# Optimization experiments

Hardware: AMD Instinct MI355X
Metric: run time of the kernel (lower is better)

Reference implementation:

```python
import jax, jax.numpy as jnp
import numpy as np

B, M, K = 8, 2048, 64          # clouds, points per cloud, max neighbors
C_IN, C_OUT, R = 64, 64, 0.2   # channels, radius
BN_EPS = 1e-5                  # BatchNorm eval: running_mean=0, running_var=1


def _bn(y, g, b):
    # eval-mode BatchNorm1d with running stats (0, 1)
    return g * y * (1.0 / jnp.sqrt(1.0 + BN_EPS)) + b


def _lin_init(key, fan_in, shape):
    s = 1.0 / np.sqrt(fan_in)
    return jax.random.uniform(key, shape, jnp.float32, -s, s)


def setup_inputs() -> dict:
    key = jax.random.key(0)
    ks = jax.random.split(key, 16)
    N = B * M
    pos = jax.random.uniform(ks[0], (N, 3), jnp.float32)
    x = jax.random.normal(ks[1], (N, C_IN), jnp.float32)
    nrm = jax.random.normal(ks[2], (N, 3), jnp.float32)
    normal = nrm / jnp.linalg.norm(nrm, axis=-1, keepdims=True)
    batch = jnp.repeat(jnp.arange(B, dtype=jnp.int32), M)
    return {
        "x": x, "pos": pos, "normal": normal, "batch": batch,
        # PointTransformerConv linear layers (value / key / query)
        "lin_w": _lin_init(ks[3], C_IN, (C_IN, C_OUT)),
        "lin_b": _lin_init(ks[4], C_IN, (C_OUT,)),
        "lin_src_w": _lin_init(ks[5], C_IN, (C_IN, C_OUT)),
        "lin_src_b": _lin_init(ks[6], C_IN, (C_OUT,)),
        "lin_dst_w": _lin_init(ks[7], C_IN, (C_IN, C_OUT)),
        "lin_dst_b": _lin_init(ks[8], C_IN, (C_OUT,)),
        # pos_nn = MLP([6, C_OUT]): Linear -> BN -> ReLU (Dropout off in eval)
        "pos_w": _lin_init(ks[9], 6, (6, C_OUT)),
        "pos_b": _lin_init(ks[10], 6, (C_OUT,)),
        "pos_g": jnp.ones((C_OUT,), jnp.float32),
        "pos_bt": jnp.zeros((C_OUT,), jnp.float32),
        # attn_nn = MLP([C_OUT, C_OUT])
        "attn_w": _lin_init(ks[11], C_OUT, (C_OUT, C_OUT)),
        "attn_b": _lin_init(ks[12], C_OUT, (C_OUT,)),
        "attn_g": jnp.ones((C_OUT,), jnp.float32),
        "attn_bt": jnp.zeros((C_OUT,), jnp.float32),
    }


def _forward(x, pos, normal, lin_w, lin_b, lin_src_w, lin_src_b,
             lin_dst_w, lin_dst_b, pos_w, pos_b, pos_g, pos_bt,
             attn_w, attn_b, attn_g, attn_bt):
    xb = x.reshape(B, M, C_IN)
    pb = pos.reshape(B, M, 3)
    nb = normal.reshape(B, M, 3)

    # radius(pos, pos, r, batch, batch, max_num_neighbors=K):
    # per-cloud pairwise sq-distances -> K nearest, masked to d <= r.
    d2 = jnp.sum((pb[:, :, None, :] - pb[:, None, :, :]) ** 2, axis=-1)  # [B,M,M]
    neg_d2, idx = jax.lax.top_k(-d2, K)                                   # [B,M,K]
    mask = (-neg_d2) <= R * R                                             # self always valid

    gather = jax.vmap(lambda a, i: a[i])  # per-cloud gather: [M,C],[M,K] -> [M,K,C]

    v = xb @ lin_w + lin_b          # value   [B,M,C]
    kf = xb @ lin_src_w + lin_src_b # key     [B,M,C]
    q = xb @ lin_dst_w + lin_dst_b  # query   [B,M,C]

    vj = gather(v, idx)             # [B,M,K,C]
    kj = gather(kf, idx)
    pj = gather(pb, idx)            # [B,M,K,3]
    nj = gather(nb, idx)

    rel = jnp.concatenate([pb[:, :, None, :] - pj,
                           nb[:, :, None, :] - nj], axis=-1)  # [B,M,K,6]
    delta = jax.nn.relu(_bn(rel @ pos_w + pos_b, pos_g, pos_bt))  # [B,M,K,C]

    alpha = jax.nn.relu(_bn((q[:, :, None, :] - kj + delta) @ attn_w + attn_b,
                            attn_g, attn_bt))                     # [B,M,K,C]
    alpha = jnp.where(mask[..., None], alpha, -jnp.inf)
    w = jax.nn.softmax(alpha, axis=2)                              # softmax over neighbors

    out = jnp.sum(w * (vj + delta), axis=2)                        # [B,M,C]
    return out.reshape(B * M, C_OUT)


def reference(x, pos, normal, batch, lin_w, lin_b, lin_src_w, lin_src_b,
              lin_dst_w, lin_dst_b, pos_w, pos_b, pos_g, pos_bt,
              attn_w, attn_b, attn_g, attn_bt):
    del batch  # batch ids are block-contiguous: encoded by the [B,M] reshape
    return _forward(x, pos, normal, lin_w, lin_b, lin_src_w, lin_src_b,
                    lin_dst_w, lin_dst_b, pos_w, pos_b, pos_g, pos_bt,
                    attn_w, attn_b, attn_g, attn_bt)
```

## Files before the change

kernel.cpp:

```cpp
#include <hip/hip_runtime.h>
#include <math.h>

#define BB 8
#define MM 2048
#define KK 64
#define CC 64
#define NTOT (BB*MM)
#define R2 0.04f
#define CAP 256

typedef _Float16 h8 __attribute__((ext_vector_type(8)));
typedef _Float16 h4 __attribute__((ext_vector_type(4)));
typedef float f32x4 __attribute__((ext_vector_type(4)));

__device__ __forceinline__ int swz(int row, int col) {
  return (row << 6) + ((((col >> 3) ^ (row & 7)) << 3) | (col & 7));
}

__device__ __forceinline__ unsigned long long shfl_xor_u64(unsigned long long x, int off) {
  int lo = __shfl_xor((int)(unsigned)(x & 0xFFFFFFFFull), off, 64);
  int hi = __shfl_xor((int)(unsigned)(x >> 32), off, 64);
  return (((unsigned long long)(unsigned)hi) << 32) | (unsigned)lo;
}

__device__ __forceinline__ unsigned long long wave_min_u64(unsigned long long x) {
#pragma unroll
  for (int off = 32; off; off >>= 1) {
    unsigned long long o = shfl_xor_u64(x, off);
    x = (o < x) ? o : x;
  }
  return x;
}

__device__ __forceinline__ unsigned long long wave_max_u64(unsigned long long x) {
#pragma unroll
  for (int off = 32; off; off >>= 1) {
    unsigned long long o = shfl_xor_u64(x, off);
    x = (o > x) ? o : x;
  }
  return x;
}

__global__ __launch_bounds__(256) void prep_w(const float* __restrict__ attn_w,
                                              const float* __restrict__ pos_w,
                                              unsigned short* __restrict__ w_img,
                                              unsigned short* __restrict__ pw_img) {
  const int idx = blockIdx.x * 256 + threadIdx.x;
  if (idx < 4096) {
    const int d = idx >> 6, cc = idx & 63;
    const float v = attn_w[idx];
    w_img[swz(cc, d)] = __builtin_bit_cast(unsigned short, (_Float16)v);
  }
  if (idx < 64 * 24) {
    const int col = idx / 24, k = idx - col * 24;
    const float v = (k < 6) ? pos_w[k * 64 + col] : 0.f;
    pw_img[idx] = __builtin_bit_cast(unsigned short, (_Float16)v);
  }
}

__global__ __launch_bounds__(256) void proj_kernel(
    const float* __restrict__ x,
    const float* __restrict__ w0, const float* __restrict__ b0,
    const float* __restrict__ w1, const float* __restrict__ b1,
    const float* __restrict__ w2, const float* __restrict__ b2,
    float* __restrict__ o0, float* __restrict__ o1, float* __restrict__ o2) {
  __shared__ float xs[64 * 64];
  __shared__ float wss[64 * 64];
  const int tid = threadIdx.x;
  const int r0 = blockIdx.x << 6;
  const float* w; const float* bv; float* o;
  if (blockIdx.y == 0)      { w = w0; bv = b0; o = o0; }
  else if (blockIdx.y == 1) { w = w1; bv = b1; o = o1; }
  else                      { w = w2; bv = b2; o = o2; }
  for (int i = tid; i < 4096; i += 256) {
    xs[i]  = x[(size_t)r0 * 64 + i];
    wss[i] = w[i];
  }
  __syncthreads();
  const int c = tid & 63, rg = tid >> 6;
  float acc[16];
#pragma unroll
  for (int r = 0; r < 16; ++r) acc[r] = 0.f;
  for (int k = 0; k < 64; ++k) {
    const float wvv = wss[(k << 6) + c];
#pragma unroll
    for (int r = 0; r < 16; ++r)
      acc[r] = fmaf(xs[((rg * 16 + r) << 6) + k], wvv, acc[r]);
  }
  const float bb = bv[c];
#pragma unroll
  for (int r = 0; r < 16; ++r)
    o[(size_t)(r0 + rg * 16 + r) * 64 + c] = acc[r] + bb;
}

__global__ __launch_bounds__(256) void knn_kernel(const float* __restrict__ pos,
                                                  unsigned* __restrict__ nbr) {
  __shared__ float spos[MM * 3];
  __shared__ unsigned long long slist[4][CAP];
  const int bidx = blockIdx.x;
  const int b = bidx >> 9;
  const int qblk = bidx & 511;
  const int tid = threadIdx.x;
  const float* pc = pos + (size_t)b * MM * 3;
  for (int i = tid; i < MM * 3; i += 256) spos[i] = pc[i];
  __syncthreads();
  const int wv = tid >> 6, lane = tid & 63;
  const int q = (qblk << 2) + wv;
  const float qx = spos[q * 3 + 0], qy = spos[q * 3 + 1], qz = spos[q * 3 + 2];
  unsigned bits[32];
  unsigned cnt = 0;
#pragma unroll
  for (int i = 0; i < 32; ++i) {
    const int j = lane + (i << 6);
    const float dx = qx - spos[j * 3 + 0];
    const float dy = qy - spos[j * 3 + 1];
    const float dz = qz - spos[j * 3 + 2];
    const float d2 = __fadd_rn(__fadd_rn(__fmul_rn(dx, dx), __fmul_rn(dy, dy)), __fmul_rn(dz, dz));
    const unsigned bt = __float_as_uint(d2);
    bits[i] = bt;
    const bool val = (d2 <= R2);
    const unsigned long long mb = __ballot(val);
    if (val) {
      const unsigned off = cnt + (unsigned)__popcll(mb & ((1ull << lane) - 1ull));
      if (off < CAP) slist[wv][off] = (((unsigned long long)bt) << 32) | (unsigned)j;
    }
    cnt += (unsigned)__popcll(mb);
  }
  __syncthreads();
  unsigned outv;
  if (cnt <= 64u) {
    if (lane < (int)cnt) outv = ((unsigned)slist[wv][lane]) | 0x80000000u;
    else                 outv = 0u;
  } else if (cnt <= (unsigned)CAP) {
    unsigned long long s0, s1, s2, s3, t;
    s0 = (lane       < (int)cnt) ? slist[wv][lane      ] : ~0ull;
    s1 = (lane + 64  < (int)cnt) ? slist[wv][lane + 64 ] : ~0ull;
    s2 = (lane + 128 < (int)cnt) ? slist[wv][lane + 128] : ~0ull;
    s3 = (lane + 192 < (int)cnt) ? slist[wv][lane + 192] : ~0ull;
    if (s1 < s0) { t = s0; s0 = s1; s1 = t; }
    if (s3 < s2) { t = s2; s2 = s3; s3 = t; }
    if (s2 < s0) { t = s0; s0 = s2; s2 = t; }
    if (s3 < s1) { t = s1; s1 = s3; s3 = t; }
    if (s2 < s1) { t = s1; s1 = s2; s2 = t; }
    if (cnt <= 128u) {
      const int pops = (int)cnt - 64;
      int rl = (cnt > (unsigned)lane) ? (int)((cnt - (unsigned)lane + 63u) >> 6) : 0;
      if (rl > 4) rl = 4;
      int ti = rl - 1;
      for (int p = 0; p < pops; ++p) {
        const unsigned long long mx =
            (ti == 3) ? s3 : (ti == 2) ? s2 : (ti == 1) ? s1 : (ti == 0) ? s0 : 0ull;
        const unsigned long long g = wave_max_u64(mx);
        if (ti >= 0 && mx == g) ti--;
      }
      const int c = ti + 1;
      const unsigned long long b0 = __ballot(c & 1);
      const unsigned long long b1 = __ballot(c & 2);
      const unsigned long long b2 = __ballot(c & 4);
      const unsigned long long lm = (1ull << lane) - 1ull;
      const int pre = __popcll(b0 & lm) + 2 * __popcll(b1 & lm) + 4 * __popcll(b2 & lm);
      if (c > 0) slist[wv][pre + 0] = s0;
      if (c > 1) slist[wv][pre + 1] = s1;
      if (c > 2) slist[wv][pre + 2] = s2;
      if (c > 3) slist[wv][pre + 3] = s3;
      __asm volatile("s_waitcnt lgkmcnt(0)" ::: "memory");
      outv = ((unsigned)slist[wv][lane]) | 0x80000000u;
    } else {
      unsigned long long my = 0;
      for (int it = 0; it < 64; ++it) {
        const unsigned long long gg = wave_min_u64(s0);
        if (lane == it) my = gg;
        if (s0 == gg) { s0 = s1; s1 = s2; s2 = s3; s3 = ~0ull; }
      }
      outv = ((unsigned)my) | 0x80000000u;
    }
  } else {
    unsigned long long cur = ~0ull;
#pragma unroll
    for (int i = 0; i < 32; ++i) {
      const unsigned long long k = (((unsigned long long)bits[i]) << 32) | (unsigned)(lane + (i << 6));
      cur = (k < cur) ? k : cur;
    }
    unsigned long long my = 0;
    for (int it = 0; it < 64; ++it) {
      const unsigned long long gg = wave_min_u64(cur);
      if (lane == it) my = gg;
      if (cur == gg) {
        cur = ~0ull;
#pragma unroll
        for (int i = 0; i < 32; ++i) {
          const unsigned long long k = (((unsigned long long)bits[i]) << 32) | (unsigned)(lane + (i << 6));
          if (k > gg && k < cur) cur = k;
        }
      }
    }
    const float d2s = __uint_as_float((unsigned)(my >> 32));
    outv = ((unsigned)my) | ((d2s <= R2) ? 0x80000000u : 0u);
  }
  nbr[((size_t)(b * MM + q)) * 64 + lane] = outv;
}

__global__ __launch_bounds__(256, 4) void ptc_kernel(
    const float* __restrict__ pos, const float* __restrict__ nrm,
    const float* __restrict__ vv, const float* __restrict__ kf, const float* __restrict__ qq,
    const unsigned* __restrict__ nbr,
    const unsigned short* __restrict__ w_img, const unsigned short* __restrict__ pw_img,
    const float* __restrict__ pos_b, const float* __restrict__ pos_g, const float* __restrict__ pos_bt,
    const float* __restrict__ attn_b, const float* __restrict__ attn_g, const float* __restrict__ attn_bt,
    float* __restrict__ out) {
  __shared__ __align__(16) unsigned short s_w[4096];
  __shared__ __align__(16) unsigned short s_thi[4096];
  __shared__ __align__(16) unsigned short s_pw[64 * 24];
  __shared__ __align__(16) unsigned short s_relh[64 * 24];
  __shared__ unsigned s_sel[64];
  const int qi = blockIdx.x;
  const int b = qi >> 11;
  const int tid = threadIdx.x;
  const int wv = tid >> 6, lane = tid & 63;
  const int lrow = lane >> 4, lcol = lane & 15;
  const int col = (wv << 4) + lcol;
  const float bninv = 1.0f / sqrtf(1.0f + 1e-5f);

  {
    const uint4* wi = (const uint4*)w_img;
    uint4* sw = (uint4*)s_w;
#pragma unroll
    for (int i = 0; i < 2; ++i) sw[tid + 256 * i] = wi[tid + 256 * i];
    if (tid < 192) ((uint4*)s_pw)[tid] = ((const uint4*)pw_img)[tid];
  }
  if (tid < 64) {
    const unsigned s = nbr[(size_t)qi * 64 + tid];
    s_sel[tid] = s;
    const int j = (int)(s & 0x7FFFFFFFu);
    const int jg = (b << 11) + j;
    h8 hv;
    hv[0] = (_Float16)(pos[(size_t)qi * 3 + 0] - pos[(size_t)jg * 3 + 0]);
    hv[1] = (_Float16)(pos[(size_t)qi * 3 + 1] - pos[(size_t)jg * 3 + 1]);
    hv[2] = (_Float16)(pos[(size_t)qi * 3 + 2] - pos[(size_t)jg * 3 + 2]);
    hv[3] = (_Float16)(nrm[(size_t)qi * 3 + 0] - nrm[(size_t)jg * 3 + 0]);
    hv[4] = (_Float16)(nrm[(size_t)qi * 3 + 1] - nrm[(size_t)jg * 3 + 1]);
    hv[5] = (_Float16)(nrm[(size_t)qi * 3 + 2] - nrm[(size_t)jg * 3 + 2]);
    hv[6] = (_Float16)0.f; hv[7] = (_Float16)0.f;
    *(h8*)&s_relh[tid * 24] = hv;
    h8 zz = (h8)(_Float16)0.f;
    *(h8*)&s_relh[tid * 24 + 8] = zz;
  }
  __syncthreads();

  f32x4 dacc[4];
  {
    const h4 bpw = *(const h4*)&s_pw[col * 24 + (lrow << 2)];
#pragma unroll
    for (int mt = 0; mt < 4; ++mt) {
      const h4 ar = *(const h4*)&s_relh[((mt << 4) + lcol) * 24 + (lrow << 2)];
      dacc[mt] = __builtin_amdgcn_mfma_f32_16x16x16f16(ar, bpw, (f32x4){0.f, 0.f, 0.f, 0.f}, 0, 0, 0);
    }
  }

  float def[16];
  unsigned selv[16];
  {
    const float pb = pos_b[col], pg = pos_g[col], pbt = pos_bt[col];
    const float qvc = qq[(size_t)qi * 64 + col];
#pragma unroll
    for (int mt = 0; mt < 4; ++mt) {
#pragma unroll
      for (int r = 0; r < 4; ++r) {
        const int i = (mt << 2) + r;
        const int n = (mt << 4) + (lrow << 2) + r;
        const float de = fmaxf(pg * (dacc[mt][r] + pb) * bninv + pbt, 0.f);
        def[i] = de;
        const unsigned s = s_sel[n];
        selv[i] = s;
        const int j = (int)(s & 0x7FFFFFFFu);
        const float kv = kf[(((size_t)((b << 11) + j)) << 6) + col];
        const float t = qvc - kv + de;
        s_thi[swz(n, col)] = __builtin_bit_cast(unsigned short, (_Float16)t);
      }
    }
  }
  __syncthreads();

  f32x4 acc[4];
#pragma unroll
  for (int mt = 0; mt < 4; ++mt) acc[mt] = (f32x4){0.f, 0.f, 0.f, 0.f};
#pragma unroll
  for (int ks = 0; ks < 2; ++ks) {
    const int kc = lrow + (ks << 2);
    const h8 bh = *(const h8*)&s_w[(col << 6) + ((kc ^ (col & 7)) << 3)];
#pragma unroll
    for (int mt = 0; mt < 4; ++mt) {
      const int m = (mt << 4) + lcol;
      const h8 ah = *(const h8*)&s_thi[(m << 6) + ((kc ^ (m & 7)) << 3)];
      acc[mt] = __builtin_amdgcn_mfma_f32_16x16x32_f16(ah, bh, acc[mt], 0, 0, 0);
    }
  }

  const float ab = attn_b[col], ag = attn_g[col], abt = attn_bt[col];
  float a[16];
  float pm = -INFINITY;
#pragma unroll
  for (int mt = 0; mt < 4; ++mt) {
#pragma unroll
    for (int r = 0; r < 4; ++r) {
      const int i = (mt << 2) + r;
      const float al = fmaxf(ag * (acc[mt][r] + ab) * bninv + abt, 0.f);
      const float av = (selv[i] >> 31) ? al : -INFINITY;
      a[i] = av;
      pm = fmaxf(pm, av);
    }
  }
  pm = fmaxf(pm, __shfl_xor(pm, 16, 64));
  pm = fmaxf(pm, __shfl_xor(pm, 32, 64));
  float ps = 0.f;
#pragma unroll
  for (int i = 0; i < 16; ++i) {
    const float e = __expf(a[i] - pm);
    a[i] = e;
    ps += e;
  }
  ps += __shfl_xor(ps, 16, 64);
  ps += __shfl_xor(ps, 32, 64);

  float o = 0.f;
#pragma unroll
  for (int i = 0; i < 16; ++i) {
    const int j = (int)(selv[i] & 0x7FFFFFFFu);
    const float vj = vv[(((size_t)((b << 11) + j)) << 6) + col];
    o = fmaf(a[i], vj + def[i], o);
  }
  o += __shfl_xor(o, 16, 64);
  o += __shfl_xor(o, 32, 64);
  if (lrow == 0) out[(size_t)qi * 64 + col] = o * (1.0f / ps);
}

extern "C" void kernel_launch(void* const* d_in, const int* in_sizes, int n_in,
                              void* d_out, int out_size, void* d_ws, size_t ws_size,
                              hipStream_t stream) {
  const float* x      = (const float*)d_in[0];
  const float* pos    = (const float*)d_in[1];
  const float* nrm    = (const float*)d_in[2];
  const float* lin_w  = (const float*)d_in[4];
  const float* lin_b  = (const float*)d_in[5];
  const float* lsw    = (const float*)d_in[6];
  const float* lsb    = (const float*)d_in[7];
  const float* ldw    = (const float*)d_in[8];
  const float* ldb    = (const float*)d_in[9];
  const float* pos_w  = (const float*)d_in[10];
  const float* pos_b  = (const float*)d_in[11];
  const float* pos_g  = (const float*)d_in[12];
  const float* pos_bt = (const float*)d_in[13];
  const float* attn_w = (const float*)d_in[14];
  const float* attn_b = (const float*)d_in[15];
  const float* attn_g = (const float*)d_in[16];
  const float* attn_bt= (const float*)d_in[17];
  float* out = (float*)d_out;

  float* wsf = (float*)d_ws;
  float* v   = wsf;
  float* kf  = wsf + (size_t)NTOT * 64;
  float* qv  = wsf + (size_t)2 * NTOT * 64;
  unsigned* nbr = (unsigned*)(wsf + (size_t)3 * NTOT * 64);
  unsigned short* w_img  = (unsigned short*)(wsf + (size_t)4 * NTOT * 64);
  unsigned short* pw_img = w_img + 4096;

  prep_w<<<16, 256, 0, stream>>>(attn_w, pos_w, w_img, pw_img);
  proj_kernel<<<dim3(NTOT / 64, 3), 256, 0, stream>>>(
      x, lin_w, lin_b, lsw, lsb, ldw, ldb, v, kf, qv);
  knn_kernel<<<BB * (MM / 4), 256, 0, stream>>>(pos, nbr);
  ptc_kernel<<<NTOT, 256, 0, stream>>>(
      pos, nrm, v, kf, qv, nbr, w_img, pw_img,
      pos_b, pos_g, pos_bt,
      attn_b, attn_g, attn_bt, out);
}
```

Measured before the change: 135.5 us.

## Use split-fp16 MFMA for projections and stage gathered neighbor rows in LDS

```diff
diff --git a/kernel.cpp b/kernel.cpp
--- a/kernel.cpp
+++ b/kernel.cpp
@@ -41,56 +41,123 @@
   return x;
 }
 
-__global__ __launch_bounds__(256) void prep_w(const float* __restrict__ attn_w,
-                                              const float* __restrict__ pos_w,
-                                              unsigned short* __restrict__ w_img,
-                                              unsigned short* __restrict__ pw_img) {
+__global__ __launch_bounds__(256) void prep_w(
+    const float* __restrict__ attn_w, const float* __restrict__ pos_w,
+    const float* __restrict__ lin_w, const float* __restrict__ lsw, const float* __restrict__ ldw,
+    const float* __restrict__ pos_b, const float* __restrict__ pos_g, const float* __restrict__ pos_bt,
+    const float* __restrict__ attn_b, const float* __restrict__ attn_g, const float* __restrict__ attn_bt,
+    unsigned short* __restrict__ w_img, unsigned short* __restrict__ pw_img,
+    unsigned short* __restrict__ pj_img, float* __restrict__ bnc) {
   const int idx = blockIdx.x * 256 + threadIdx.x;
+  const float bninv = 1.0f / sqrtf(1.0f + 1e-5f);
   if (idx < 4096) {
     const int d = idx >> 6, cc = idx & 63;
-    const float v = attn_w[idx];
-    w_img[swz(cc, d)] = __builtin_bit_cast(unsigned short, (_Float16)v);
+    const int sp = swz(cc, d);
+    w_img[sp] = __builtin_bit_cast(unsigned short, (_Float16)attn_w[idx]);
+    const float v0 = lin_w[idx];
+    const _Float16 h0 = (_Float16)v0;
+    pj_img[sp] = __builtin_bit_cast(unsigned short, h0);
+    pj_img[4096 + sp] = __builtin_bit_cast(unsigned short, (_Float16)(v0 - (float)h0));
+    const float v1 = lsw[idx];
+    const _Float16 h1 = (_Float16)v1;
+    pj_img[8192 + sp] = __builtin_bit_cast(unsigned short, h1);
+    pj_img[12288 + sp] = __builtin_bit_cast(unsigned short, (_Float16)(v1 - (float)h1));
+    const float v2 = ldw[idx];
+    const _Float16 h2 = (_Float16)v2;
+    pj_img[16384 + sp] = __builtin_bit_cast(unsigned short, h2);
+    pj_img[20480 + sp] = __builtin_bit_cast(unsigned short, (_Float16)(v2 - (float)h2));
   }
   if (idx < 64 * 24) {
     const int col = idx / 24, k = idx - col * 24;
     const float v = (k < 6) ? pos_w[k * 64 + col] : 0.f;
     pw_img[idx] = __builtin_bit_cast(unsigned short, (_Float16)v);
   }
-}
-
-__global__ __launch_bounds__(256) void proj_kernel(
-    const float* __restrict__ x,
-    const float* __restrict__ w0, const float* __restrict__ b0,
-    const float* __restrict__ w1, const float* __restrict__ b1,
-    const float* __restrict__ w2, const float* __restrict__ b2,
+  if (idx < 64) {
+    const float pA = pos_g[idx] * bninv;
+    bnc[idx] = pA;
+    bnc[64 + idx] = pA * pos_b[idx] + pos_bt[idx];
+    const float aA = attn_g[idx] * bninv;
+    bnc[128 + idx] = aA;
+    bnc[192 + idx] = aA * attn_b[idx] + attn_bt[idx];
+  }
+}
+
+__global__ __launch_bounds__(256, 2) void proj_mfma(
+    const float* __restrict__ x, const unsigned short* __restrict__ pj_img,
+    const float* __restrict__ b0, const float* __restrict__ b1, const float* __restrict__ b2,
     float* __restrict__ o0, float* __restrict__ o1, float* __restrict__ o2) {
-  __shared__ float xs[64 * 64];
-  __shared__ float wss[64 * 64];
+  __shared__ __align__(16) unsigned short s_xh[4096];
+  __shared__ __align__(16) unsigned short s_xl[4096];
+  __shared__ __align__(16) unsigned short s_w6[6 * 4096];
   const int tid = threadIdx.x;
   const int r0 = blockIdx.x << 6;
-  const float* w; const float* bv; float* o;
-  if (blockIdx.y == 0)      { w = w0; bv = b0; o = o0; }
-  else if (blockIdx.y == 1) { w = w1; bv = b1; o = o1; }
-  else                      { w = w2; bv = b2; o = o2; }
-  for (int i = tid; i < 4096; i += 256) {
-    xs[i]  = x[(size_t)r0 * 64 + i];
-    wss[i] = w[i];
-  }
-  __syncthreads();
-  const int c = tid & 63, rg = tid >> 6;
-  float acc[16];
-#pragma unroll
-  for (int r = 0; r < 16; ++r) acc[r] = 0.f;
-  for (int k = 0; k < 64; ++k) {
-    const float wvv = wss[(k << 6) + c];
-#pragma unroll
-    for (int r = 0; r < 16; ++r)
-      acc[r] = fmaf(xs[((rg * 16 + r) << 6) + k], wvv, acc[r]);
-  }
-  const float bb = bv[c];
-#pragma unroll
-  for (int r = 0; r < 16; ++r)
-    o[(size_t)(r0 + rg * 16 + r) * 64 + c] = acc[r] + bb;
+  for (int i = tid; i < 3072; i += 256)
+    ((uint4*)s_w6)[i] = ((const uint4*)pj_img)[i];
+  {
+    const int row = tid >> 2, seg = tid & 3;
+    const float* xr = x + (((size_t)(r0 + row)) << 6) + (seg << 4);
+    float xb[16];
+#pragma unroll
+    for (int q = 0; q < 4; ++q) *(float4*)&xb[q * 4] = ((const float4*)xr)[q];
+    h8 c0h, c1h, c0l, c1l;
+#pragma unroll
+    for (int e = 0; e < 8; ++e) {
+      const _Float16 h0 = (_Float16)xb[e];
+      c0h[e] = h0; c0l[e] = (_Float16)(xb[e] - (float)h0);
+      const _Float16 h1 = (_Float16)xb[e + 8];
+      c1h[e] = h1; c1l[e] = (_Float16)(xb[e + 8] - (float)h1);
+    }
+    const int base = row << 6;
+    const int oi0 = base + ((((seg << 1) | 0) ^ (row & 7)) << 3);
+    const int oi1 = base + ((((seg << 1) | 1) ^ (row & 7)) << 3);
+    *(h8*)&s_xh[oi0] = c0h; *(h8*)&s_xh[oi1] = c1h;
+    *(h8*)&s_xl[oi0] = c0l; *(h8*)&s_xl[oi1] = c1l;
+  }
+  __syncthreads();
+  const int wv = tid >> 6, lane = tid & 63, lrow = lane >> 4, lcol = lane & 15;
+  const int col = (wv << 4) + lcol;
+  f32x4 acc[3][4];
+#pragma unroll
+  for (int o = 0; o < 3; ++o)
+#pragma unroll
+    for (int mt = 0; mt < 4; ++mt) acc[o][mt] = (f32x4){0.f, 0.f, 0.f, 0.f};
+#pragma unroll
+  for (int ks = 0; ks < 2; ++ks) {
+    const int kc = lrow + (ks << 2);
+    const int boff = (col << 6) + ((kc ^ (col & 7)) << 3);
+    const h8 bh0 = *(const h8*)&s_w6[boff];
+    const h8 bl0 = *(const h8*)&s_w6[4096 + boff];
+    const h8 bh1 = *(const h8*)&s_w6[8192 + boff];
+    const h8 bl1 = *(const h8*)&s_w6[12288 + boff];
+    const h8 bh2 = *(const h8*)&s_w6[16384 + boff];
+    const h8 bl2 = *(const h8*)&s_w6[20480 + boff];
+#pragma unroll
+    for (int mt = 0; mt < 4; ++mt) {
+      const int m = (mt << 4) + lcol;
+      const int aoff = (m << 6) + ((kc ^ (m & 7)) << 3);
+      const h8 ah = *(const h8*)&s_xh[aoff];
+      const h8 al = *(const h8*)&s_xl[aoff];
+      acc[0][mt] = __builtin_amdgcn_mfma_f32_16x16x32_f16(ah, bh0, acc[0][mt], 0, 0, 0);
+      acc[0][mt] = __builtin_amdgcn_mfma_f32_16x16x32_f16(al, bh0, acc[0][mt], 0, 0, 0);
+      acc[0][mt] = __builtin_amdgcn_mfma_f32_16x16x32_f16(ah, bl0, acc[0][mt], 0, 0, 0);
+      acc[1][mt] = __builtin_amdgcn_mfma_f32_16x16x32_f16(ah, bh1, acc[1][mt], 0, 0, 0);
+      acc[1][mt] = __builtin_amdgcn_mfma_f32_16x16x32_f16(al, bh1, acc[1][mt], 0, 0, 0);
+      acc[1][mt] = __builtin_amdgcn_mfma_f32_16x16x32_f16(ah, bl1, acc[1][mt], 0, 0, 0);
+      acc[2][mt] = __builtin_amdgcn_mfma_f32_16x16x32_f16(ah, bh2, acc[2][mt], 0, 0, 0);
+      acc[2][mt] = __builtin_amdgcn_mfma_f32_16x16x32_f16(al, bh2, acc[2][mt], 0, 0, 0);
+      acc[2][mt] = __builtin_amdgcn_mfma_f32_16x16x32_f16(ah, bl2, acc[2][mt], 0, 0, 0);
+    }
+  }
+  const float bb0 = b0[col], bb1 = b1[col], bb2 = b2[col];
+#pragma unroll
+  for (int mt = 0; mt < 4; ++mt)
+#pragma unroll
+    for (int r = 0; r < 4; ++r) {
+      const size_t gi = (((size_t)(r0 + (mt << 4) + (lrow << 2) + r)) << 6) + col;
+      o0[gi] = acc[0][mt][r] + bb0;
+      o1[gi] = acc[1][mt][r] + bb1;
+      o2[gi] = acc[2][mt][r] + bb2;
+    }
 }
 
 __global__ __launch_bounds__(256) void knn_kernel(const float* __restrict__ pos,
@@ -102,7 +169,8 @@
   const int qblk = bidx & 511;
   const int tid = threadIdx.x;
   const float* pc = pos + (size_t)b * MM * 3;
-  for (int i = tid; i < MM * 3; i += 256) spos[i] = pc[i];
+  for (int i = tid; i < MM * 3 / 4; i += 256)
+    ((float4*)spos)[i] = ((const float4*)pc)[i];
   __syncthreads();
   const int wv = tid >> 6, lane = tid & 63;
   const int q = (qblk << 2) + wv;
@@ -205,11 +273,11 @@
     const float* __restrict__ vv, const float* __restrict__ kf, const float* __restrict__ qq,
     const unsigned* __restrict__ nbr,
     const unsigned short* __restrict__ w_img, const unsigned short* __restrict__ pw_img,
-    const float* __restrict__ pos_b, const float* __restrict__ pos_g, const float* __restrict__ pos_bt,
-    const float* __restrict__ attn_b, const float* __restrict__ attn_g, const float* __restrict__ attn_bt,
+    const float* __restrict__ bnc,
     float* __restrict__ out) {
   __shared__ __align__(16) unsigned short s_w[4096];
-  __shared__ __align__(16) unsigned short s_thi[4096];
+  __shared__ __align__(16) unsigned short s_kt[4096];
+  __shared__ __align__(16) unsigned short s_vv[4096];
   __shared__ __align__(16) unsigned short s_pw[64 * 24];
   __shared__ __align__(16) unsigned short s_relh[64 * 24];
   __shared__ unsigned s_sel[64];
@@ -219,19 +287,43 @@
   const int wv = tid >> 6, lane = tid & 63;
   const int lrow = lane >> 4, lcol = lane & 15;
   const int col = (wv << 4) + lcol;
-  const float bninv = 1.0f / sqrtf(1.0f + 1e-5f);
-
+
+  if (tid < 64) s_sel[tid] = nbr[(size_t)qi * 64 + tid];
   {
     const uint4* wi = (const uint4*)w_img;
     uint4* sw = (uint4*)s_w;
-#pragma unroll
-    for (int i = 0; i < 2; ++i) sw[tid + 256 * i] = wi[tid + 256 * i];
+    sw[tid] = wi[tid];
+    sw[tid + 256] = wi[tid + 256];
     if (tid < 192) ((uint4*)s_pw)[tid] = ((const uint4*)pw_img)[tid];
   }
+  __syncthreads();
+
+  {
+    const int row = tid >> 2, seg = tid & 3;
+    const int j = (int)(s_sel[row] & 0x7FFFFFFFu);
+    const size_t rb = (((size_t)((b << 11) + j)) << 6) + (seg << 4);
+    const float* kr = kf + rb;
+    const float* vr = vv + rb;
+    float kb[16], vb[16];
+#pragma unroll
+    for (int q = 0; q < 4; ++q) {
+      *(float4*)&kb[q * 4] = ((const float4*)kr)[q];
+      *(float4*)&vb[q * 4] = ((const float4*)vr)[q];
+    }
+    h8 kc0, kc1, vc0, vc1;
+#pragma unroll
+    for (int e = 0; e < 8; ++e) {
+      kc0[e] = (_Float16)kb[e]; kc1[e] = (_Float16)kb[e + 8];
+      vc0[e] = (_Float16)vb[e]; vc1[e] = (_Float16)vb[e + 8];
+    }
+    const int base = row << 6;
+    const int oi0 = base + ((((seg << 1) | 0) ^ (row & 7)) << 3);
+    const int oi1 = base + ((((seg << 1) | 1) ^ (row & 7)) << 3);
+    *(h8*)&s_kt[oi0] = kc0; *(h8*)&s_kt[oi1] = kc1;
+    *(h8*)&s_vv[oi0] = vc0; *(h8*)&s_vv[oi1] = vc1;
+  }
   if (tid < 64) {
-    const unsigned s = nbr[(size_t)qi * 64 + tid];
-    s_sel[tid] = s;
-    const int j = (int)(s & 0x7FFFFFFFu);
+    const int j = (int)(s_sel[tid] & 0x7FFFFFFFu);
     const int jg = (b << 11) + j;
     h8 hv;
     hv[0] = (_Float16)(pos[(size_t)qi * 3 + 0] - pos[(size_t)jg * 3 + 0]);
@@ -257,26 +349,22 @@
     }
   }
 
+  const float pA = bnc[col], pB = bnc[64 + col];
+  const float aA = bnc[128 + col], aB = bnc[192 + col];
+  const float qvc = qq[(size_t)qi * 64 + col];
   float def[16];
-  unsigned selv[16];
-  {
-    const float pb = pos_b[col], pg = pos_g[col], pbt = pos_bt[col];
-    const float qvc = qq[(size_t)qi * 64 + col];
-#pragma unroll
-    for (int mt = 0; mt < 4; ++mt) {
-#pragma unroll
-      for (int r = 0; r < 4; ++r) {
-        const int i = (mt << 2) + r;
-        const int n = (mt << 4) + (lrow << 2) + r;
-        const float de = fmaxf(pg * (dacc[mt][r] + pb) * bninv + pbt, 0.f);
-        def[i] = de;
-        const unsigned s = s_sel[n];
-        selv[i] = s;
-        const int j = (int)(s & 0x7FFFFFFFu);
-        const float kv = kf[(((size_t)((b << 11) + j)) << 6) + col];
-        const float t = qvc - kv + de;
-        s_thi[swz(n, col)] = __builtin_bit_cast(unsigned short, (_Float16)t);
-      }
+#pragma unroll
+  for (int mt = 0; mt < 4; ++mt) {
+#pragma unroll
+    for (int r = 0; r < 4; ++r) {
+      const int i = (mt << 2) + r;
+      const int n = (mt << 4) + (lrow << 2) + r;
+      const int hw = swz(n, col);
+      const float kv = (float)*(const _Float16*)&s_kt[hw];
+      const float de = fmaxf(fmaf(pA, dacc[mt][r], pB), 0.f);
+      def[i] = de;
+      const float t = qvc - kv + de;
+      *(_Float16*)&s_kt[hw] = (_Float16)t;
     }
   }
   __syncthreads();
@@ -291,21 +379,22 @@
 #pragma unroll
     for (int mt = 0; mt < 4; ++mt) {
       const int m = (mt << 4) + lcol;
-      const h8 ah = *(const h8*)&s_thi[(m << 6) + ((kc ^ (m & 7)) << 3)];
+      const h8 ah = *(const h8*)&s_kt[(m << 6) + ((kc ^ (m & 7)) << 3)];
       acc[mt] = __builtin_amdgcn_mfma_f32_16x16x32_f16(ah, bh, acc[mt], 0, 0, 0);
     }
   }
 
-  const float ab = attn_b[col], ag = attn_g[col], abt = attn_bt[col];
   float a[16];
   float pm = -INFINITY;
 #pragma unroll
   for (int mt = 0; mt < 4; ++mt) {
+    const uint4 s4 = *(const uint4*)&s_sel[(mt << 4) + (lrow << 2)];
+    const unsigned sv[4] = {s4.x, s4.y, s4.z, s4.w};
 #pragma unroll
     for (int r = 0; r < 4; ++r) {
       const int i = (mt << 2) + r;
-      const float al = fmaxf(ag * (acc[mt][r] + ab) * bninv + abt, 0.f);
-      const float av = (selv[i] >> 31) ? al : -INFINITY;
+      const float al = fmaxf(fmaf(aA, acc[mt][r], aB), 0.f);
+      const float av = (sv[r] >> 31) ? al : -INFINITY;
       a[i] = av;
       pm = fmaxf(pm, av);
     }
@@ -324,10 +413,14 @@
 
   float o = 0.f;
 #pragma unroll
-  for (int i = 0; i < 16; ++i) {
-    const int j = (int)(selv[i] & 0x7FFFFFFFu);
-    const float vj = vv[(((size_t)((b << 11) + j)) << 6) + col];
-    o = fmaf(a[i], vj + def[i], o);
+  for (int mt = 0; mt < 4; ++mt) {
+#pragma unroll
+    for (int r = 0; r < 4; ++r) {
+      const int i = (mt << 2) + r;
+      const int n = (mt << 4) + (lrow << 2) + r;
+      const float vj = (float)*(const _Float16*)&s_vv[swz(n, col)];
+      o = fmaf(a[i], vj + def[i], o);
+    }
   }
   o += __shfl_xor(o, 16, 64);
   o += __shfl_xor(o, 32, 64);
@@ -363,13 +456,15 @@
   unsigned* nbr = (unsigned*)(wsf + (size_t)3 * NTOT * 64);
   unsigned short* w_img  = (unsigned short*)(wsf + (size_t)4 * NTOT * 64);
   unsigned short* pw_img = w_img + 4096;
-
-  prep_w<<<16, 256, 0, stream>>>(attn_w, pos_w, w_img, pw_img);
-  proj_kernel<<<dim3(NTOT / 64, 3), 256, 0, stream>>>(
-      x, lin_w, lin_b, lsw, lsb, ldw, ldb, v, kf, qv);
+  unsigned short* pj_img = pw_img + 1536;
+  float* bnc = (float*)(pj_img + 24576);
+
+  prep_w<<<16, 256, 0, stream>>>(attn_w, pos_w, lin_w, lsw, ldw,
+                                 pos_b, pos_g, pos_bt, attn_b, attn_g, attn_bt,
+                                 w_img, pw_img, pj_img, bnc);
+  proj_mfma<<<NTOT / 64, 256, 0, stream>>>(
+      x, pj_img, lin_b, lsb, ldb, v, kf, qv);
   knn_kernel<<<BB * (MM / 4), 256, 0, stream>>>(pos, nbr);
   ptc_kernel<<<NTOT, 256, 0, stream>>>(
-      pos, nrm, v, kf, qv, nbr, w_img, pw_img,
-      pos_b, pos_g, pos_bt,
-      attn_b, attn_g, attn_bt, out);
-}
+      pos, nrm, v, kf, qv, nbr, w_img, pw_img, bnc, out);
+}
```

Result: faster. 131.4 us (-3.1%).
